# Optimization experiments

Hardware: AMD Instinct MI355X
Metric: run time of the kernel (lower is better)

Reference implementation:

```python
import jax, jax.numpy as jnp
import numpy as np
from jax.ops import segment_sum, segment_max

N, E, F_IN, H1, H2, HEADS, OUT, G = 50000, 800000, 64, 64, 64, 4, 32, 500

def setup_inputs() -> dict:
    key = jax.random.key(0)
    ks = jax.random.split(key, 12)
    x = jax.random.normal(ks[0], (N, F_IN), dtype=jnp.float32)
    edge_index = jax.random.randint(ks[1], (2, E), 0, N, dtype=jnp.int64)
    batch = jnp.sort(jax.random.randint(ks[2], (N,), 0, G, dtype=jnp.int64))
    def glorot(k, shape):
        fan = shape[0] + shape[-1]
        return jax.random.uniform(k, shape, jnp.float32, -1.0, 1.0) * jnp.sqrt(6.0 / fan)
    return {
        "x": x,
        "edge_index": edge_index,
        "batch": batch,
        "gcn_W": glorot(ks[3], (F_IN, H1)),
        "gcn_b": jnp.zeros((H1,), jnp.float32),
        "gat_W": glorot(ks[4], (H1, HEADS * H2)),
        "att_src": glorot(ks[5], (HEADS, H2)),
        "att_dst": glorot(ks[6], (HEADS, H2)),
        "gat_b": jnp.zeros((HEADS * H2,), jnp.float32),
        "out_W": glorot(ks[7], (HEADS * H2, OUT)),
        "out_b": jnp.zeros((OUT,), jnp.float32),
    }

def reference(x, edge_index, batch, gcn_W, gcn_b, gat_W, att_src, att_dst, gat_b, out_W, out_b):
    n = x.shape[0]
    loop = jnp.arange(n)
    # edges with self-loops: src (j) -> dst (i), PyG convention
    src = jnp.concatenate([edge_index[0], loop])
    dst = jnp.concatenate([edge_index[1], loop])

    # ---- GCNConv: symmetric normalized scatter-add ----
    h = x @ gcn_W                                            # [N, H1]
    deg = segment_sum(jnp.ones_like(dst, dtype=h.dtype), dst, num_segments=n)
    dinv = jnp.where(deg > 0, jax.lax.rsqrt(deg), 0.0)       # deg^{-1/2}
    norm = dinv[src] * dinv[dst]                             # [E']
    h = segment_sum(norm[:, None] * h[src], dst, num_segments=n) + gcn_b
    h = jax.nn.relu(h)

    # ---- GATConv: per-edge attention + segment softmax over dst ----
    g = (h @ gat_W).reshape(n, HEADS, H2)                    # [N, H, C]
    a_s = jnp.einsum('nhc,hc->nh', g, att_src)               # [N, H]
    a_d = jnp.einsum('nhc,hc->nh', g, att_dst)
    e = jax.nn.leaky_relu(a_s[src] + a_d[dst], 0.2)          # [E', H]
    m = segment_max(e, dst, num_segments=n)                  # every node has a self-loop
    e = jnp.exp(e - m[dst])
    denom = segment_sum(e, dst, num_segments=n)
    alpha = e / denom[dst]                                   # [E', H]
    agg = segment_sum(alpha[:, :, None] * g[src], dst, num_segments=n)  # [N, H, C]
    z = jax.nn.relu(agg.reshape(n, HEADS * H2) + gat_b)

    # ---- global mean pool over graphs + output linear ----
    cnt = segment_sum(jnp.ones((n,), z.dtype), batch, num_segments=G)
    pooled = segment_sum(z, batch, num_segments=G) / jnp.maximum(cnt, 1.0)[:, None]
    return pooled @ out_W + out_b
```

## Files before the change

kernel.cpp:

```cpp
#include <hip/hip_runtime.h>
#include <math.h>

#define NN 50000
#define NE 800000
#define NEP (NE + NN)
#define NGRAPH 500
#define NOUT 32
#define NBLK 196

typedef _Float16 half4 __attribute__((ext_vector_type(4)));
typedef _Float16 half8 __attribute__((ext_vector_type(8)));
typedef _Float16 half2v __attribute__((ext_vector_type(2)));

__device__ __forceinline__ float lrelu(float x) { return x > 0.f ? x : 0.2f * x; }
__device__ __forceinline__ half2v bch2(float f) { return __builtin_bit_cast(half2v, f); }

__device__ __forceinline__ unsigned fkey(float f) {
    unsigned b = __float_as_uint(f);
    return (b & 0x80000000u) ? ~b : (b | 0x80000000u);
}
__device__ __forceinline__ float funkey(unsigned k) {
    unsigned b = (k & 0x80000000u) ? (k & 0x7fffffffu) : ~k;
    return __uint_as_float(b);
}


__global__ void k_count(const int* __restrict__ dst, int* __restrict__ cnt,
                        int* __restrict__ pos) {
    int e = blockIdx.x * blockDim.x + threadIdx.x;
    if (e < NE) pos[e] = atomicAdd(&cnt[dst[e]], 1);
}

__global__ __launch_bounds__(256) void k_scan1(const int* __restrict__ cnt, int* __restrict__ bsum,
                                               float* __restrict__ pool, float* __restrict__ cnt_g,
                                               unsigned* __restrict__ gmaxU,
                                               const float* __restrict__ gat_W,
                                               const float* __restrict__ att_src,
                                               const float* __restrict__ att_dst,
                                               float* __restrict__ UV,
                                               _Float16* __restrict__ W16T) {
    __shared__ int buf[256];
    int gid = blockIdx.x * 256 + threadIdx.x;
    int v = (gid < NN) ? (cnt[gid] + 1) : 0;
    buf[threadIdx.x] = v;
    for (int j = gid; j < NGRAPH * 256; j += NBLK * 256) pool[j] = 0.f;
    if (gid < NGRAPH) cnt_g[gid] = 0.f;
    if (gid < 4) gmaxU[gid] = 0u;
    for (int j = gid; j < 64 * 256; j += NBLK * 256) {
        int c = j >> 6, f = j & 63;
        W16T[j] = (_Float16)gat_W[f * 256 + c];
    }
    if (gid < 512) {
        int f = gid >> 3, o = gid & 7, h = o & 3;
        const float* av = (o < 4) ? att_src : att_dst;
        float s = 0.f;
#pragma unroll 8
        for (int c = 0; c < 64; ++c) s += gat_W[f * 256 + h * 64 + c] * av[h * 64 + c];
        UV[gid] = s;
    }
    __syncthreads();
    for (int off = 128; off; off >>= 1) {
        if (threadIdx.x < off) buf[threadIdx.x] += buf[threadIdx.x + off];
        __syncthreads();
    }
    if (threadIdx.x == 0) bsum[blockIdx.x] = buf[0];
}

__global__ __launch_bounds__(256) void k_scan3(const int* __restrict__ cnt,
                                               const int* __restrict__ bsum,
                                               int* __restrict__ row_ptr,
                                               float* __restrict__ dinv,
                                               int* __restrict__ col) {
    __shared__ int sb[256];
    __shared__ int buf[256];
    int tid = threadIdx.x;
    int bv = (tid < NBLK) ? bsum[tid] : 0;
    sb[tid] = bv;
    __syncthreads();
    for (int off = 1; off < 256; off <<= 1) {
        int t = (tid >= off) ? sb[tid - off] : 0;
        __syncthreads();
        sb[tid] += t;
        __syncthreads();
    }
    int blockoff = (blockIdx.x == 0) ? 0 : sb[blockIdx.x - 1];
    int i = blockIdx.x * 256 + tid;
    int v = (i < NN) ? (cnt[i] + 1) : 0;
    buf[tid] = v;
    __syncthreads();
    for (int off = 1; off < 256; off <<= 1) {
        int t = (tid >= off) ? buf[tid - off] : 0;
        __syncthreads();
        buf[tid] += t;
        __syncthreads();
    }
    if (i < NN) {
        int rp = blockoff + buf[tid] - v;
        row_ptr[i] = rp;
        dinv[i] = rsqrtf((float)(cnt[i] + 1));
        col[rp] = i;
    }
    if (i == 0) row_ptr[NN] = NEP;
}

__global__ void k_fill(const int* __restrict__ src, const int* __restrict__ dst,
                       const int* __restrict__ row_ptr, const int* __restrict__ pos,
                       int* __restrict__ col) {
    int idx = blockIdx.x * blockDim.x + threadIdx.x;
    if (idx < NE) {
        int d = dst[idx];
        col[row_ptr[d] + 1 + pos[idx]] = src[idx];
    }
}


__global__ __launch_bounds__(256) void k_gemm64(const float* __restrict__ A,
                                                const float* __restrict__ B,
                                                const float* __restrict__ dinv,
                                                _Float16* __restrict__ C16, int n) {
    __shared__ float Bs[64 * 64];
    __shared__ float As[64 * 68];
    int tid = threadIdx.x;
    int rb = blockIdx.x * 64;
    for (int i = tid; i < 1024; i += 256) ((float4*)Bs)[i] = ((const float4*)B)[i];
    for (int i = tid; i < 1024; i += 256) {
        int r = i >> 4, c = i & 15;
        int row = rb + r; if (row >= n) row = n - 1;
        ((float4*)As)[r * 17 + c] = ((const float4*)A)[(size_t)row * 16 + c];
    }
    __syncthreads();
    int lane = tid & 63, wv = tid >> 6;
    int fl = lane & 15, sub = lane >> 4;
    int r0 = wv * 16 + sub * 4;
    const float4* Bs4 = (const float4*)Bs;
    float4 acc0 = {0,0,0,0}, acc1 = {0,0,0,0}, acc2 = {0,0,0,0}, acc3 = {0,0,0,0};
#pragma unroll 4
    for (int k = 0; k < 64; ++k) {
        float4 b4 = Bs4[k * 16 + fl];
        float a0 = As[(r0 + 0) * 68 + k];
        float a1 = As[(r0 + 1) * 68 + k];
        float a2 = As[(r0 + 2) * 68 + k];
        float a3 = As[(r0 + 3) * 68 + k];
        acc0.x += a0 * b4.x; acc0.y += a0 * b4.y; acc0.z += a0 * b4.z; acc0.w += a0 * b4.w;
        acc1.x += a1 * b4.x; acc1.y += a1 * b4.y; acc1.z += a1 * b4.z; acc1.w += a1 * b4.w;
        acc2.x += a2 * b4.x; acc2.y += a2 * b4.y; acc2.z += a2 * b4.z; acc2.w += a2 * b4.w;
        acc3.x += a3 * b4.x; acc3.y += a3 * b4.y; acc3.z += a3 * b4.z; acc3.w += a3 * b4.w;
    }
    int row = rb + r0;
    float d0 = dinv[row + 0 < n ? row + 0 : n - 1];
    float d1 = dinv[row + 1 < n ? row + 1 : n - 1];
    float d2 = dinv[row + 2 < n ? row + 2 : n - 1];
    float d3 = dinv[row + 3 < n ? row + 3 : n - 1];
    half4 h0, h1, h2, h3;
    h0.x=(_Float16)(acc0.x*d0); h0.y=(_Float16)(acc0.y*d0); h0.z=(_Float16)(acc0.z*d0); h0.w=(_Float16)(acc0.w*d0);
    h1.x=(_Float16)(acc1.x*d1); h1.y=(_Float16)(acc1.y*d1); h1.z=(_Float16)(acc1.z*d1); h1.w=(_Float16)(acc1.w*d1);
    h2.x=(_Float16)(acc2.x*d2); h2.y=(_Float16)(acc2.y*d2); h2.z=(_Float16)(acc2.z*d2); h2.w=(_Float16)(acc2.w*d2);
    h3.x=(_Float16)(acc3.x*d3); h3.y=(_Float16)(acc3.y*d3); h3.z=(_Float16)(acc3.z*d3); h3.w=(_Float16)(acc3.w*d3);
    if (row + 0 < n) ((half4*)(C16 + (size_t)(row + 0) * 64))[fl] = h0;
    if (row + 1 < n) ((half4*)(C16 + (size_t)(row + 1) * 64))[fl] = h1;
    if (row + 2 < n) ((half4*)(C16 + (size_t)(row + 2) * 64))[fl] = h2;
    if (row + 3 < n) ((half4*)(C16 + (size_t)(row + 3) * 64))[fl] = h3;
}


__global__ __launch_bounds__(256) void k_gcn_agg(const _Float16* __restrict__ hxs16,
                                                 const int* __restrict__ row_ptr,
                                                 const int* __restrict__ col,
                                                 const float* __restrict__ dinv,
                                                 const float* __restrict__ bias,
                                                 const float* __restrict__ UV,
                                                 _Float16* __restrict__ h16,
                                                 float* __restrict__ a_s,
                                                 float* __restrict__ a_d) {
    int wid = (blockIdx.x * blockDim.x + threadIdx.x) >> 6;
    int lane = threadIdx.x & 63;
    if (wid >= NN) return;
    int slot = lane >> 3;
    int fl   = lane & 7;
    int s0 = row_ptr[wid], s1 = row_ptr[wid + 1];
    float di = dinv[wid];
    const half8* hx8 = (const half8*)hxs16;
    float a0 = 0.f, a1 = 0.f, a2 = 0.f, a3 = 0.f;
    float a4 = 0.f, a5 = 0.f, a6 = 0.f, a7 = 0.f;
    int k = s0 + slot;
    for (; k + 8 < s1; k += 16) {
        int i0 = col[k], i1 = col[k + 8];
        half8 v0 = hx8[(size_t)i0 * 8 + fl];
        half8 v1 = hx8[(size_t)i1 * 8 + fl];
        a0 += (float)v0[0] + (float)v1[0];
        a1 += (float)v0[1] + (float)v1[1];
        a2 += (float)v0[2] + (float)v1[2];
        a3 += (float)v0[3] + (float)v1[3];
        a4 += (float)v0[4] + (float)v1[4];
        a5 += (float)v0[5] + (float)v1[5];
        a6 += (float)v0[6] + (float)v1[6];
        a7 += (float)v0[7] + (float)v1[7];
    }
    for (; k < s1; k += 8) {
        half8 v = hx8[(size_t)col[k] * 8 + fl];
        a0 += (float)v[0]; a1 += (float)v[1];
        a2 += (float)v[2]; a3 += (float)v[3];
        a4 += (float)v[4]; a5 += (float)v[5];
        a6 += (float)v[6]; a7 += (float)v[7];
    }
#define RED8(x) x += __shfl_xor(x, 8); x += __shfl_xor(x, 16); x += __shfl_xor(x, 32);
    RED8(a0) RED8(a1) RED8(a2) RED8(a3) RED8(a4) RED8(a5) RED8(a6) RED8(a7)
#undef RED8
    float4 bbA = ((const float4*)bias)[2 * fl];
    float4 bbB = ((const float4*)bias)[2 * fl + 1];
    float z0 = fmaxf(a0 * di + bbA.x, 0.f);
    float z1 = fmaxf(a1 * di + bbA.y, 0.f);
    float z2 = fmaxf(a2 * di + bbA.z, 0.f);
    float z3 = fmaxf(a3 * di + bbA.w, 0.f);
    float z4 = fmaxf(a4 * di + bbB.x, 0.f);
    float z5 = fmaxf(a5 * di + bbB.y, 0.f);
    float z6 = fmaxf(a6 * di + bbB.z, 0.f);
    float z7 = fmaxf(a7 * di + bbB.w, 0.f);
    if (slot == 0) {
        half8 z;
        z[0] = (_Float16)z0; z[1] = (_Float16)z1; z[2] = (_Float16)z2; z[3] = (_Float16)z3;
        z[4] = (_Float16)z4; z[5] = (_Float16)z5; z[6] = (_Float16)z6; z[7] = (_Float16)z7;
        ((half8*)(h16 + (size_t)wid * 64))[fl] = z;
    }
    int f0 = fl * 8;
    float val = z0 * UV[(f0 + 0) * 8 + slot] + z1 * UV[(f0 + 1) * 8 + slot]
              + z2 * UV[(f0 + 2) * 8 + slot] + z3 * UV[(f0 + 3) * 8 + slot]
              + z4 * UV[(f0 + 4) * 8 + slot] + z5 * UV[(f0 + 5) * 8 + slot]
              + z6 * UV[(f0 + 6) * 8 + slot] + z7 * UV[(f0 + 7) * 8 + slot];
    val += __shfl_xor(val, 1);
    val += __shfl_xor(val, 2);
    val += __shfl_xor(val, 4);
    if (fl == 0) {
        if (slot < 4) a_s[wid * 4 + slot] = val;
        else          a_d[wid * 4 + (slot - 4)] = val;
    }
}


__global__ __launch_bounds__(256) void k_gmax(const float* __restrict__ a_s,
                                              unsigned* __restrict__ gmaxU) {
    __shared__ unsigned sm[4];
    int tid = threadIdx.x;
    if (tid < 4) sm[tid] = 0u;
    __syncthreads();
    float mx = -1e30f, my = -1e30f, mz = -1e30f, mw = -1e30f;
    int stride = gridDim.x * 256;
    for (int n = blockIdx.x * 256 + tid; n < NN; n += stride) {
        float4 v = ((const float4*)a_s)[n];
        mx = fmaxf(mx, v.x); my = fmaxf(my, v.y);
        mz = fmaxf(mz, v.z); mw = fmaxf(mw, v.w);
    }
    atomicMax(&sm[0], fkey(mx)); atomicMax(&sm[1], fkey(my));
    atomicMax(&sm[2], fkey(mz)); atomicMax(&sm[3], fkey(mw));
    __syncthreads();
    if (tid < 4) atomicMax(&gmaxU[tid], sm[tid]);
}


__global__ __launch_bounds__(256) void k_gat_h(const _Float16* __restrict__ h16,
                                               const float* __restrict__ a_s,
                                               const float* __restrict__ a_d,
                                               const int* __restrict__ row_ptr,
                                               const int* __restrict__ col,
                                               const unsigned* __restrict__ gmaxU,
                                               _Float16* __restrict__ aggH) {
    int tid = threadIdx.x;
    int wv = tid >> 6, lane = tid & 63;
    int wid = blockIdx.x * 4 + wv;
    int slot = lane >> 4;
    int fl = lane & 15;

    int s0 = row_ptr[wid], s1 = row_ptr[wid + 1];
    float4 ad4 = ((const float4*)a_d)[wid];
    float M0 = lrelu(funkey(gmaxU[0]) + ad4.x);
    float M1 = lrelu(funkey(gmaxU[1]) + ad4.y);
    float M2 = lrelu(funkey(gmaxU[2]) + ad4.z);
    float M3 = lrelu(funkey(gmaxU[3]) + ad4.w);
    const half4* h4 = (const half4*)h16;
    const float4* as4 = (const float4*)a_s;

    float t0 = 1e-30f, t1 = 1e-30f, t2 = 1e-30f, t3 = 1e-30f;
    float4 A0 = {0,0,0,0}, A1 = {0,0,0,0}, A2 = {0,0,0,0}, A3 = {0,0,0,0};

    int k = s0 + slot;
    for (; k + 4 < s1; k += 8) {
        int ia = col[k], ib = col[k + 4];
        float4 ea = as4[ia];
        float4 eb = as4[ib];
        half4 va = h4[(size_t)ia * 16 + fl];
        half4 vb = h4[(size_t)ib * 16 + fl];
        float wa0 = __expf(lrelu(ea.x + ad4.x) - M0);
        float wa1 = __expf(lrelu(ea.y + ad4.y) - M1);
        float wa2 = __expf(lrelu(ea.z + ad4.z) - M2);
        float wa3 = __expf(lrelu(ea.w + ad4.w) - M3);
        float wb0 = __expf(lrelu(eb.x + ad4.x) - M0);
        float wb1 = __expf(lrelu(eb.y + ad4.y) - M1);
        float wb2 = __expf(lrelu(eb.z + ad4.z) - M2);
        float wb3 = __expf(lrelu(eb.w + ad4.w) - M3);
        t0 += wa0 + wb0; t1 += wa1 + wb1; t2 += wa2 + wb2; t3 += wa3 + wb3;
        float vax = (float)va.x, vay = (float)va.y, vaz = (float)va.z, vaw = (float)va.w;
        float vbx = (float)vb.x, vby = (float)vb.y, vbz = (float)vb.z, vbw = (float)vb.w;
        A0.x += wa0 * vax + wb0 * vbx; A0.y += wa0 * vay + wb0 * vby;
        A0.z += wa0 * vaz + wb0 * vbz; A0.w += wa0 * vaw + wb0 * vbw;
        A1.x += wa1 * vax + wb1 * vbx; A1.y += wa1 * vay + wb1 * vby;
        A1.z += wa1 * vaz + wb1 * vbz; A1.w += wa1 * vaw + wb1 * vbw;
        A2.x += wa2 * vax + wb2 * vbx; A2.y += wa2 * vay + wb2 * vby;
        A2.z += wa2 * vaz + wb2 * vbz; A2.w += wa2 * vaw + wb2 * vbw;
        A3.x += wa3 * vax + wb3 * vbx; A3.y += wa3 * vay + wb3 * vby;
        A3.z += wa3 * vaz + wb3 * vbz; A3.w += wa3 * vaw + wb3 * vbw;
    }
    if (k < s1) {
        int ia = col[k];
        float4 ea = as4[ia];
        half4 va = h4[(size_t)ia * 16 + fl];
        float wa0 = __expf(lrelu(ea.x + ad4.x) - M0);
        float wa1 = __expf(lrelu(ea.y + ad4.y) - M1);
        float wa2 = __expf(lrelu(ea.z + ad4.z) - M2);
        float wa3 = __expf(lrelu(ea.w + ad4.w) - M3);
        t0 += wa0; t1 += wa1; t2 += wa2; t3 += wa3;
        float vax = (float)va.x, vay = (float)va.y, vaz = (float)va.z, vaw = (float)va.w;
        A0.x += wa0 * vax; A0.y += wa0 * vay; A0.z += wa0 * vaz; A0.w += wa0 * vaw;
        A1.x += wa1 * vax; A1.y += wa1 * vay; A1.z += wa1 * vaz; A1.w += wa1 * vaw;
        A2.x += wa2 * vax; A2.y += wa2 * vay; A2.z += wa2 * vaz; A2.w += wa2 * vaw;
        A3.x += wa3 * vax; A3.y += wa3 * vay; A3.z += wa3 * vaz; A3.w += wa3 * vaw;
    }
#define REDX(x) x += __shfl_xor(x, 16); x += __shfl_xor(x, 32);
    REDX(t0) REDX(t1) REDX(t2) REDX(t3)
    REDX(A0.x) REDX(A0.y) REDX(A0.z) REDX(A0.w)
    REDX(A1.x) REDX(A1.y) REDX(A1.z) REDX(A1.w)
    REDX(A2.x) REDX(A2.y) REDX(A2.z) REDX(A2.w)
    REDX(A3.x) REDX(A3.y) REDX(A3.z) REDX(A3.w)
#undef REDX
    float rsel = slot == 0 ? t0 : slot == 1 ? t1 : slot == 2 ? t2 : t3;
    float4 Asel = slot == 0 ? A0 : slot == 1 ? A1 : slot == 2 ? A2 : A3;
    float r = 1.f / rsel;
    half4 o;
    o.x = (_Float16)(Asel.x * r); o.y = (_Float16)(Asel.y * r);
    o.z = (_Float16)(Asel.z * r); o.w = (_Float16)(Asel.w * r);
    ((half4*)(aggH + (size_t)wid * 256))[lane] = o;
}


__global__ __launch_bounds__(256) void k_post2(const _Float16* __restrict__ aggH,
                                               const _Float16* __restrict__ W16T,
                                               const float* __restrict__ gat_b,
                                               const int* __restrict__ batch,
                                               float* __restrict__ pool,
                                               float* __restrict__ cnt_g) {
    int tid = threadIdx.x;
    int lane = tid & 63;
    int wv = __builtin_amdgcn_readfirstlane(tid >> 6);
    int h = blockIdx.y;
    int c = h * 64 + lane;
    const float4* wp = (const float4*)(W16T + (size_t)c * 64);
    float4 Wb[8];
#pragma unroll
    for (int i = 0; i < 8; ++i) Wb[i] = wp[i];
    float gb = gat_b[c];

    int rbeg = (blockIdx.x * 4 + wv) * 32;
    int rend = rbeg + 32; if (rend > NN) rend = NN;

    float psum = 0.f;
    int curb = -1, rcnt = 0;
#pragma unroll 2
    for (int row = rbeg; row < rend; ++row) {
        int b = batch[row];
        if (b != curb) {
            if (curb >= 0) {
                atomicAdd(&pool[(size_t)curb * 256 + c], psum);
                if (h == 0 && lane == 0) atomicAdd(&cnt_g[curb], (float)rcnt);
            }
            psum = 0.f; rcnt = 0; curb = b;
        }
        const float4* ap = (const float4*)(aggH + (size_t)row * 256 + h * 64);
        float4 Ab[8];
#pragma unroll
        for (int i = 0; i < 8; ++i) Ab[i] = ap[i];
        float ac0 = 0.f, ac1 = 0.f, ac2 = 0.f, ac3 = 0.f;
#pragma unroll
        for (int i = 0; i < 8; ++i) {
            ac0 = __builtin_amdgcn_fdot2(bch2(Ab[i].x), bch2(Wb[i].x), ac0, false);
            ac1 = __builtin_amdgcn_fdot2(bch2(Ab[i].y), bch2(Wb[i].y), ac1, false);
            ac2 = __builtin_amdgcn_fdot2(bch2(Ab[i].z), bch2(Wb[i].z), ac2, false);
            ac3 = __builtin_amdgcn_fdot2(bch2(Ab[i].w), bch2(Wb[i].w), ac3, false);
        }
        float acc = (ac0 + ac1) + (ac2 + ac3);
        psum += fmaxf(acc + gb, 0.f);
        ++rcnt;
    }
    if (curb >= 0) {
        atomicAdd(&pool[(size_t)curb * 256 + c], psum);
        if (h == 0 && lane == 0) atomicAdd(&cnt_g[curb], (float)rcnt);
    }
}


__global__ void k_out(const float* __restrict__ pool, const float* __restrict__ cnt_g,
                      const float* __restrict__ W, const float* __restrict__ b,
                      float* __restrict__ out) {
    int idx = blockIdx.x * blockDim.x + threadIdx.x;
    if (idx >= NGRAPH * NOUT) return;
    int gg = idx >> 5, o = idx & 31;
    float c = cnt_g[gg];
    c = c > 1.f ? c : 1.f;
    float rinv = 1.f / c;
    const float* p = pool + (size_t)gg * 256;
    float acc = 0.f;
#pragma unroll 8
    for (int f = 0; f < 256; ++f) acc += p[f] * W[f * 32 + o];
    out[idx] = acc * rinv + b[o];
}


extern "C" void kernel_launch(void* const* d_in, const int* in_sizes, int n_in,
                              void* d_out, int out_size, void* d_ws, size_t ws_size,
                              hipStream_t stream) {
    const float* x       = (const float*)d_in[0];
    const int*   eidx    = (const int*)d_in[1];
    const int*   batch   = (const int*)d_in[2];
    const float* gcn_W   = (const float*)d_in[3];
    const float* gcn_b   = (const float*)d_in[4];
    const float* gat_W   = (const float*)d_in[5];
    const float* att_src = (const float*)d_in[6];
    const float* att_dst = (const float*)d_in[7];
    const float* gat_b   = (const float*)d_in[8];
    const float* out_W   = (const float*)d_in[9];
    const float* out_b   = (const float*)d_in[10];
    float* out = (float*)d_out;

    const int* src = eidx;
    const int* dst = eidx + NE;

    size_t off = 0;
    auto carve = [&](size_t bytes) -> char* {
        char* p = (char*)d_ws + off;
        off += (bytes + 255) & ~(size_t)255;
        return p;
    };
    int*      cnt     = (int*)carve(NN * sizeof(int));
    int*      pos     = (int*)carve((size_t)NE * sizeof(int));
    int*      row_ptr = (int*)carve((NN + 1) * sizeof(int));
    int*      bsum    = (int*)carve(256 * sizeof(int));
    int*      colb    = (int*)carve((size_t)NEP * sizeof(int));
    float*    dinv    = (float*)carve(NN * sizeof(float));
    _Float16* hx16    = (_Float16*)carve((size_t)NN * 64 * sizeof(_Float16));
    _Float16* h16     = (_Float16*)carve((size_t)NN * 64 * sizeof(_Float16));
    _Float16* aggH16  = (_Float16*)carve((size_t)NN * 256 * sizeof(_Float16));
    float*    a_s     = (float*)carve((size_t)NN * 4 * sizeof(float));
    float*    a_d     = (float*)carve((size_t)NN * 4 * sizeof(float));
    float*    UV      = (float*)carve(64 * 8 * sizeof(float));
    _Float16* W16T    = (_Float16*)carve(64 * 256 * sizeof(_Float16));
    unsigned* gmaxU   = (unsigned*)carve(4 * sizeof(unsigned));
    float*    pool    = (float*)carve((size_t)NGRAPH * 256 * sizeof(float));
    float*    cnt_g   = (float*)carve(NGRAPH * sizeof(float));

    hipMemsetAsync(cnt, 0, NN * sizeof(int), stream);

    k_count<<<(NE + 255) / 256, 256, 0, stream>>>(dst, cnt, pos);
    k_scan1<<<NBLK, 256, 0, stream>>>(cnt, bsum, pool, cnt_g, gmaxU,
                                      gat_W, att_src, att_dst, UV, W16T);
    k_scan3<<<NBLK, 256, 0, stream>>>(cnt, bsum, row_ptr, dinv, colb);
    k_fill<<<(NE + 255) / 256, 256, 0, stream>>>(src, dst, row_ptr, pos, colb);

    k_gemm64<<<(NN + 63) / 64, 256, 0, stream>>>(x, gcn_W, dinv, hx16, NN);
    k_gcn_agg<<<(NN * 64 + 255) / 256, 256, 0, stream>>>(hx16, row_ptr, colb, dinv, gcn_b,
                                                         UV, h16, a_s, a_d);

    k_gmax<<<128, 256, 0, stream>>>(a_s, gmaxU);
    k_gat_h<<<NN / 4, 256, 0, stream>>>(h16, a_s, a_d, row_ptr, colb, gmaxU, aggH16);

    k_post2<<<dim3(391, 4), 256, 0, stream>>>(aggH16, W16T, gat_b, batch, pool, cnt_g);

    k_out<<<(NGRAPH * NOUT + 255) / 256, 256, 0, stream>>>(pool, cnt_g, out_W, out_b, out);
}
```

Before: 289.6 us.

## Remap GAT aggregation lanes to per-head groups with 8-wide feature loads

Reorganizes the GAT aggregation wave so each lane owns one head and eight feature columns, with two edge groups per wave instead of four edge slots covering all heads. Each lane now computes a single exp weight per edge rather than four, loads half8 vectors, and unrolls over four edges. This removes redundant per-lane exp work and shrinks the cross-lane reduction to one shuffle step. In exchange, each lane handles only two edge streams, and a_s is read as scalar loads per head instead of float4.

```diff
diff --git a/kernel.cpp b/kernel.cpp
--- a/kernel.cpp
+++ b/kernel.cpp
@@ -267,77 +267,69 @@
     int tid = threadIdx.x;
     int wv = tid >> 6, lane = tid & 63;
     int wid = blockIdx.x * 4 + wv;
-    int slot = lane >> 4;
-    int fl = lane & 15;
+    int grp  = lane >> 5;
+    int head = (lane >> 3) & 3;
+    int fl   = lane & 7;
 
     int s0 = row_ptr[wid], s1 = row_ptr[wid + 1];
-    float4 ad4 = ((const float4*)a_d)[wid];
-    float M0 = lrelu(funkey(gmaxU[0]) + ad4.x);
-    float M1 = lrelu(funkey(gmaxU[1]) + ad4.y);
-    float M2 = lrelu(funkey(gmaxU[2]) + ad4.z);
-    float M3 = lrelu(funkey(gmaxU[3]) + ad4.w);
-    const half4* h4 = (const half4*)h16;
-    const float4* as4 = (const float4*)a_s;
-
-    float t0 = 1e-30f, t1 = 1e-30f, t2 = 1e-30f, t3 = 1e-30f;
-    float4 A0 = {0,0,0,0}, A1 = {0,0,0,0}, A2 = {0,0,0,0}, A3 = {0,0,0,0};
-
-    int k = s0 + slot;
-    for (; k + 4 < s1; k += 8) {
-        int ia = col[k], ib = col[k + 4];
-        float4 ea = as4[ia];
-        float4 eb = as4[ib];
-        half4 va = h4[(size_t)ia * 16 + fl];
-        half4 vb = h4[(size_t)ib * 16 + fl];
-        float wa0 = __expf(lrelu(ea.x + ad4.x) - M0);
-        float wa1 = __expf(lrelu(ea.y + ad4.y) - M1);
-        float wa2 = __expf(lrelu(ea.z + ad4.z) - M2);
-        float wa3 = __expf(lrelu(ea.w + ad4.w) - M3);
-        float wb0 = __expf(lrelu(eb.x + ad4.x) - M0);
-        float wb1 = __expf(lrelu(eb.y + ad4.y) - M1);
-        float wb2 = __expf(lrelu(eb.z + ad4.z) - M2);
-        float wb3 = __expf(lrelu(eb.w + ad4.w) - M3);
-        t0 += wa0 + wb0; t1 += wa1 + wb1; t2 += wa2 + wb2; t3 += wa3 + wb3;
-        float vax = (float)va.x, vay = (float)va.y, vaz = (float)va.z, vaw = (float)va.w;
-        float vbx = (float)vb.x, vby = (float)vb.y, vbz = (float)vb.z, vbw = (float)vb.w;
-        A0.x += wa0 * vax + wb0 * vbx; A0.y += wa0 * vay + wb0 * vby;
-        A0.z += wa0 * vaz + wb0 * vbz; A0.w += wa0 * vaw + wb0 * vbw;
-        A1.x += wa1 * vax + wb1 * vbx; A1.y += wa1 * vay + wb1 * vby;
-        A1.z += wa1 * vaz + wb1 * vbz; A1.w += wa1 * vaw + wb1 * vbw;
-        A2.x += wa2 * vax + wb2 * vbx; A2.y += wa2 * vay + wb2 * vby;
-        A2.z += wa2 * vaz + wb2 * vbz; A2.w += wa2 * vaw + wb2 * vbw;
-        A3.x += wa3 * vax + wb3 * vbx; A3.y += wa3 * vay + wb3 * vby;
-        A3.z += wa3 * vaz + wb3 * vbz; A3.w += wa3 * vaw + wb3 * vbw;
-    }
-    if (k < s1) {
-        int ia = col[k];
-        float4 ea = as4[ia];
-        half4 va = h4[(size_t)ia * 16 + fl];
-        float wa0 = __expf(lrelu(ea.x + ad4.x) - M0);
-        float wa1 = __expf(lrelu(ea.y + ad4.y) - M1);
-        float wa2 = __expf(lrelu(ea.z + ad4.z) - M2);
-        float wa3 = __expf(lrelu(ea.w + ad4.w) - M3);
-        t0 += wa0; t1 += wa1; t2 += wa2; t3 += wa3;
-        float vax = (float)va.x, vay = (float)va.y, vaz = (float)va.z, vaw = (float)va.w;
-        A0.x += wa0 * vax; A0.y += wa0 * vay; A0.z += wa0 * vaz; A0.w += wa0 * vaw;
-        A1.x += wa1 * vax; A1.y += wa1 * vay; A1.z += wa1 * vaz; A1.w += wa1 * vaw;
-        A2.x += wa2 * vax; A2.y += wa2 * vay; A2.z += wa2 * vaz; A2.w += wa2 * vaw;
-        A3.x += wa3 * vax; A3.y += wa3 * vay; A3.z += wa3 * vaz; A3.w += wa3 * vaw;
-    }
-#define REDX(x) x += __shfl_xor(x, 16); x += __shfl_xor(x, 32);
-    REDX(t0) REDX(t1) REDX(t2) REDX(t3)
-    REDX(A0.x) REDX(A0.y) REDX(A0.z) REDX(A0.w)
-    REDX(A1.x) REDX(A1.y) REDX(A1.z) REDX(A1.w)
-    REDX(A2.x) REDX(A2.y) REDX(A2.z) REDX(A2.w)
-    REDX(A3.x) REDX(A3.y) REDX(A3.z) REDX(A3.w)
-#undef REDX
-    float rsel = slot == 0 ? t0 : slot == 1 ? t1 : slot == 2 ? t2 : t3;
-    float4 Asel = slot == 0 ? A0 : slot == 1 ? A1 : slot == 2 ? A2 : A3;
-    float r = 1.f / rsel;
-    half4 o;
-    o.x = (_Float16)(Asel.x * r); o.y = (_Float16)(Asel.y * r);
-    o.z = (_Float16)(Asel.z * r); o.w = (_Float16)(Asel.w * r);
-    ((half4*)(aggH + (size_t)wid * 256))[lane] = o;
+    float adh = a_d[wid * 4 + head];
+    float Mh = lrelu(funkey(gmaxU[head]) + adh);
+    const half8* h8 = (const half8*)h16;
+
+    float t = 1e-30f;
+    float c0 = 0.f, c1 = 0.f, c2 = 0.f, c3 = 0.f;
+    float c4 = 0.f, c5 = 0.f, c6 = 0.f, c7 = 0.f;
+
+    int k = s0 + grp;
+    for (; k + 6 < s1; k += 8) {
+        int i0 = col[k], i1 = col[k + 2], i2 = col[k + 4], i3 = col[k + 6];
+        float e0 = a_s[i0 * 4 + head];
+        float e1 = a_s[i1 * 4 + head];
+        float e2 = a_s[i2 * 4 + head];
+        float e3 = a_s[i3 * 4 + head];
+        half8 v0 = h8[(size_t)i0 * 8 + fl];
+        half8 v1 = h8[(size_t)i1 * 8 + fl];
+        half8 v2 = h8[(size_t)i2 * 8 + fl];
+        half8 v3 = h8[(size_t)i3 * 8 + fl];
+        float w0 = __expf(lrelu(e0 + adh) - Mh);
+        float w1 = __expf(lrelu(e1 + adh) - Mh);
+        float w2 = __expf(lrelu(e2 + adh) - Mh);
+        float w3 = __expf(lrelu(e3 + adh) - Mh);
+        t += (w0 + w1) + (w2 + w3);
+        c0 += w0 * (float)v0[0] + w1 * (float)v1[0] + w2 * (float)v2[0] + w3 * (float)v3[0];
+        c1 += w0 * (float)v0[1] + w1 * (float)v1[1] + w2 * (float)v2[1] + w3 * (float)v3[1];
+        c2 += w0 * (float)v0[2] + w1 * (float)v1[2] + w2 * (float)v2[2] + w3 * (float)v3[2];
+        c3 += w0 * (float)v0[3] + w1 * (float)v1[3] + w2 * (float)v2[3] + w3 * (float)v3[3];
+        c4 += w0 * (float)v0[4] + w1 * (float)v1[4] + w2 * (float)v2[4] + w3 * (float)v3[4];
+        c5 += w0 * (float)v0[5] + w1 * (float)v1[5] + w2 * (float)v2[5] + w3 * (float)v3[5];
+        c6 += w0 * (float)v0[6] + w1 * (float)v1[6] + w2 * (float)v2[6] + w3 * (float)v3[6];
+        c7 += w0 * (float)v0[7] + w1 * (float)v1[7] + w2 * (float)v2[7] + w3 * (float)v3[7];
+    }
+    for (; k < s1; k += 2) {
+        int i0 = col[k];
+        float e0 = a_s[i0 * 4 + head];
+        half8 v0 = h8[(size_t)i0 * 8 + fl];
+        float w0 = __expf(lrelu(e0 + adh) - Mh);
+        t += w0;
+        c0 += w0 * (float)v0[0]; c1 += w0 * (float)v0[1];
+        c2 += w0 * (float)v0[2]; c3 += w0 * (float)v0[3];
+        c4 += w0 * (float)v0[4]; c5 += w0 * (float)v0[5];
+        c6 += w0 * (float)v0[6]; c7 += w0 * (float)v0[7];
+    }
+    t  += __shfl_xor(t, 32);
+    c0 += __shfl_xor(c0, 32); c1 += __shfl_xor(c1, 32);
+    c2 += __shfl_xor(c2, 32); c3 += __shfl_xor(c3, 32);
+    c4 += __shfl_xor(c4, 32); c5 += __shfl_xor(c5, 32);
+    c6 += __shfl_xor(c6, 32); c7 += __shfl_xor(c7, 32);
+    if (grp == 0) {
+        float r = 1.f / t;
+        half8 o;
+        o[0] = (_Float16)(c0 * r); o[1] = (_Float16)(c1 * r);
+        o[2] = (_Float16)(c2 * r); o[3] = (_Float16)(c3 * r);
+        o[4] = (_Float16)(c4 * r); o[5] = (_Float16)(c5 * r);
+        o[6] = (_Float16)(c6 * r); o[7] = (_Float16)(c7 * r);
+        ((half8*)(aggH + (size_t)wid * 256))[head * 8 + fl] = o;
+    }
 }
 
 
```

Measured after the change: 284.4 us. No clear change (-1.8%).
